# Kernel optimization log

Hardware: AMD Instinct MI355X
Metric: run time of the kernel (lower is better)

The kernel has to match this reference:

```python
import jax, jax.numpy as jnp
import numpy as np

B, C, T, F, H, O, L = 32, 8, 64, 256, 512, 1, 2


def _gru_layer(x, h0, Wih, Whh, bih, bhh):
    # x: [N, T, Fin]; Wih: [3H, Fin]; Whh: [3H, H]
    gi = jnp.einsum('ntf,gf->ntg', x, Wih) + bih  # precompute input gates [N, T, 3H]

    def step(h, gi_t):
        gh = h @ Whh.T + bhh                      # [N, 3H]
        ir, iz, inn = jnp.split(gi_t, 3, axis=-1)
        hr, hz, hn = jnp.split(gh, 3, axis=-1)
        r = jax.nn.sigmoid(ir + hr)
        z = jax.nn.sigmoid(iz + hz)
        n = jnp.tanh(inn + r * hn)
        h = (1.0 - z) * n + z * h                 # PyTorch GRU update
        return h, h

    hT, ys = jax.lax.scan(step, h0, jnp.swapaxes(gi, 0, 1))
    return jnp.swapaxes(ys, 0, 1), hT             # [N, T, H], [N, H]


def setup_inputs() -> dict:
    key = jax.random.key(0)
    ks = jax.random.split(key, 12)
    s = 1.0 / np.sqrt(H)
    u = lambda k, shp: jax.random.uniform(k, shp, jnp.float32, -s, s)
    return {
        'x': jax.random.normal(ks[0], (B, C, T, F), jnp.float32),
        'Wih0': u(ks[1], (3 * H, F)),
        'Whh0': u(ks[2], (3 * H, H)),
        'bih0': u(ks[3], (3 * H,)),
        'bhh0': u(ks[4], (3 * H,)),
        'Wih1': u(ks[5], (3 * H, H)),
        'Whh1': u(ks[6], (3 * H, H)),
        'bih1': u(ks[7], (3 * H,)),
        'bhh1': u(ks[8], (3 * H,)),
        'fcW': u(ks[9], (O, H)),
        'fcb': u(ks[10], (O,)),
    }


def reference(x, Wih0, Whh0, bih0, bhh0, Wih1, Whh1, bih1, bhh1, fcW, fcb):
    b, c, t, f = x.shape
    xf = x.reshape(b * c, t, f)
    h0 = jnp.zeros((b * c, H), x.dtype)
    # The per-timestep Python loop in the original carries h_n, which is
    # mathematically identical to a full-sequence GRU; out after the loop is
    # the top-layer output at the final timestep.
    y0, _ = _gru_layer(xf, h0, Wih0, Whh0, bih0, bhh0)
    y1, _ = _gru_layer(y0, h0, Wih1, Whh1, bih1, bhh1)
    last = y1[:, -1, :]                           # [b*c, H]
    out = last @ fcW.T + fcb                      # [b*c, O]
    out = out.reshape(b, c, -1).squeeze(axis=2)   # O == 1 -> [b, c]
    return jnp.mean(out, axis=1)                  # [b]
```

## Files before the change

### kernel.cpp

```cpp
#include <hip/hip_runtime.h>
#include <math.h>

#define BB 32
#define CC 8
#define TT 64
#define FF 256
#define HH 512
#define G3 1536
#define NSEQ 256
#define MROWS 16384

#define SGRP 16
#define NGRP 4

typedef _Float16 f16x8 __attribute__((ext_vector_type(8)));
typedef float f32x4 __attribute__((ext_vector_type(4)));

#define TMg 128
#define TNg 128
#define TKg 16

__global__ __launch_bounds__(256) void gemm_bias(
    const float* __restrict__ A, const float* __restrict__ W,
    const float* __restrict__ bias, float* __restrict__ C,
    int M, int N, int K)
{
  __shared__ float As[TKg][TMg + 4];
  __shared__ float Ws[TKg][TNg + 4];
  const int bm = blockIdx.y * TMg;
  const int bn = blockIdx.x * TNg;
  const int tid = threadIdx.x;
  const int tx = tid & 15;
  const int ty = tid >> 4;
  float acc[8][8];
#pragma unroll
  for (int i = 0; i < 8; ++i)
#pragma unroll
    for (int j = 0; j < 8; ++j) acc[i][j] = 0.f;

  for (int k0 = 0; k0 < K; k0 += TKg) {
    __syncthreads();
#pragma unroll
    for (int i = 0; i < 8; ++i) {
      int e = i * 256 + tid;
      int r = e >> 4;
      int c = e & 15;
      As[c][r] = A[(size_t)(bm + r) * K + (k0 + c)];
      Ws[c][r] = W[(size_t)(bn + r) * K + (k0 + c)];
    }
    __syncthreads();
#pragma unroll
    for (int k = 0; k < TKg; ++k) {
      float a[8], w[8];
#pragma unroll
      for (int i = 0; i < 8; ++i) a[i] = As[k][ty * 8 + i];
#pragma unroll
      for (int j = 0; j < 8; ++j) w[j] = Ws[k][tx + 16 * j];
#pragma unroll
      for (int i = 0; i < 8; ++i)
#pragma unroll
        for (int j = 0; j < 8; ++j) acc[i][j] = fmaf(a[i], w[j], acc[i][j]);
    }
  }
#pragma unroll
  for (int i = 0; i < 8; ++i) {
    size_t m = (size_t)(bm + ty * 8 + i);
#pragma unroll
    for (int j = 0; j < 8; ++j) {
      int n = bn + tx + 16 * j;
      C[m * N + n] = acc[i][j] + bias[n];
    }
  }
}

__global__ __launch_bounds__(256) void conv16(
    const float* __restrict__ x, _Float16* __restrict__ xh, int n8)
{
  int i = blockIdx.x * 256 + threadIdx.x;
  if (i < n8) {
    float4 a = reinterpret_cast<const float4*>(x)[i * 2];
    float4 b = reinterpret_cast<const float4*>(x)[i * 2 + 1];
    f16x8 v;
    v[0] = (_Float16)a.x; v[1] = (_Float16)a.y; v[2] = (_Float16)a.z; v[3] = (_Float16)a.w;
    v[4] = (_Float16)b.x; v[5] = (_Float16)b.y; v[6] = (_Float16)b.z; v[7] = (_Float16)b.w;
    reinterpret_cast<f16x8*>(xh)[i] = v;
  }
}

__global__ __launch_bounds__(256) void pack_wih(
    const float* __restrict__ W, _Float16* __restrict__ P, int K)
{
  int id = blockIdx.x * 256 + threadIdx.x;
  int lane = id & 63;
  int kcs = K >> 5;
  int t6 = id >> 6;
  int kc = t6 % kcs;
  int tile = t6 / kcs;
  if (tile >= 96) return;
  int row = tile * 16 + (lane & 15);
  int k0 = kc * 32 + ((lane >> 4) * 8);
  const float* src = W + (size_t)row * K + k0;
  f16x8 v;
#pragma unroll
  for (int i = 0; i < 8; ++i) v[i] = (_Float16)src[i];
  *reinterpret_cast<f16x8*>(P + (size_t)id * 8) = v;
}

__global__ __launch_bounds__(256) void pack_whh(
    const float* __restrict__ W, _Float16* __restrict__ P)
{
  int id = blockIdx.x * 256 + threadIdx.x;
  int lane = id & 63;
  int kc = (id >> 6) & 15;
  int tidx = id >> 10;
  int ng = tidx / 24;
  int tl = tidx % 24;
  int g = tl >> 3, sub = tl & 7;
  int gt = g * 32 + ng * 8 + sub;
  int row = gt * 16 + (lane & 15);
  int k0 = kc * 32 + ((lane >> 4) * 8);
  const float* src = W + (size_t)row * HH + k0;
  f16x8 v;
#pragma unroll
  for (int i = 0; i < 8; ++i) v[i] = (_Float16)src[i];
  *reinterpret_cast<f16x8*>(P + (size_t)id * 8) = v;
}

__device__ __forceinline__ void gload16g(const _Float16* g, _Float16* l) {
  __builtin_amdgcn_global_load_lds(
      (const __attribute__((address_space(1))) unsigned int*)g,
      (__attribute__((address_space(3))) unsigned int*)l, 16, 0, 0);
}

__global__ __launch_bounds__(256, 2) void gemm_mfma(
    const _Float16* __restrict__ A,
    const _Float16* __restrict__ Bp,
    const float* __restrict__ bias,
    float* __restrict__ C,
    int K)
{
  __shared__ __align__(16) _Float16 As[2][128][36];
  __shared__ __align__(16) _Float16 Bs[2][8 * 512];

  const int tid = threadIdx.x;
  const int lane = tid & 63;
  const int wv = tid >> 6;
  const int wm = wv >> 1, wn = wv & 1;
  const int bnT = blockIdx.x * 8;
  const int bm = blockIdx.y * 128;
  const int kcs = K >> 5;

  const int arow = lane & 15;
  const int agrp = lane >> 4;
  const int dcol = lane & 15;
  const int mrow = (lane >> 4) * 4;

  f32x4 acc[4][4];
#pragma unroll
  for (int i = 0; i < 4; ++i)
#pragma unroll
    for (int j = 0; j < 4; ++j) acc[i][j] = (f32x4){0.f, 0.f, 0.f, 0.f};

  auto stageA = [&](int s, int b) {
#pragma unroll
    for (int p = 0; p < 2; ++p) {
      int idx = p * 256 + tid;
      int row = idx >> 2;
      int cs = idx & 3;
      f16x8 v = *reinterpret_cast<const f16x8*>(
          A + (size_t)(bm + row) * K + s * 32 + cs * 8);
      *reinterpret_cast<f16x8*>(&As[b][row][cs * 8]) = v;
    }
  };
  auto stageB = [&](int s, int b) {
#pragma unroll
    for (int q = 0; q < 2; ++q) {
      int nt = wv * 2 + q;
      const _Float16* src = Bp + ((size_t)((bnT + nt) * kcs + s) * 64 + lane) * 8;
      gload16g(src, &Bs[b][nt * 512]);
    }
  };

  stageA(0, 0);
  stageB(0, 0);
  __syncthreads();

  for (int s = 0; s < kcs; ++s) {
    const int b = s & 1;
    if (s + 1 < kcs) {
      stageA(s + 1, b ^ 1);
      stageB(s + 1, b ^ 1);
    }
    f16x8 af[4], bf[4];
#pragma unroll
    for (int mt = 0; mt < 4; ++mt)
      af[mt] = *reinterpret_cast<const f16x8*>(&As[b][wm * 64 + mt * 16 + arow][agrp * 8]);
#pragma unroll
    for (int nt = 0; nt < 4; ++nt)
      bf[nt] = *reinterpret_cast<const f16x8*>(&Bs[b][(wn * 4 + nt) * 512 + lane * 8]);
#pragma unroll
    for (int mt = 0; mt < 4; ++mt)
#pragma unroll
      for (int nt = 0; nt < 4; ++nt)
        acc[mt][nt] = __builtin_amdgcn_mfma_f32_16x16x32_f16(af[mt], bf[nt], acc[mt][nt], 0, 0, 0);
    __syncthreads();
  }

#pragma unroll
  for (int nt = 0; nt < 4; ++nt) {
    const int n = (bnT + wn * 4 + nt) * 16 + dcol;
    const float bv = bias[n];
#pragma unroll
    for (int mt = 0; mt < 4; ++mt) {
      const size_t m0 = (size_t)(bm + wm * 64 + mt * 16 + mrow);
#pragma unroll
      for (int r = 0; r < 4; ++r)
        C[(m0 + r) * G3 + n] = acc[mt][nt][r] + bv;
    }
  }
}

#define SPB2 16
#define HSTR 520

#define LOADW(buf, g)                                                            \
  {                                                                              \
    const _Float16* _s = packW +                                                 \
        (((size_t)(ng * 24 + (g) * 8 + wid)) * 16) * 512 + (size_t)lane * 8;     \
    _Pragma("unroll")                                                            \
    for (int kc = 0; kc < 16; ++kc)                                              \
      buf[kc] = *reinterpret_cast<const f16x8*>(_s + (size_t)kc * 512);          \
  }

#define MF16(buf, acc)                                                           \
  {                                                                              \
    _Pragma("unroll")                                                            \
    for (int kc = 0; kc < 16; ++kc) {                                            \
      f16x8 _ha = *reinterpret_cast<const f16x8*>(&hs[arow][kc * 32 + agrp * 8]); \
      acc = __builtin_amdgcn_mfma_f32_16x16x32_f16(_ha, buf[kc], acc, 0, 0, 0);  \
    }                                                                            \
  }

__global__ __launch_bounds__(512, 1) void gru_scan_mfma(
    const float* __restrict__ gi,
    const _Float16* __restrict__ packW,
    const float* __restrict__ bhh,
    float* __restrict__ hfin,
    _Float16* __restrict__ yout,
    _Float16* __restrict__ hx,
    unsigned int* __restrict__ flags)
{
  __shared__ __align__(16) _Float16 hs[SPB2][HSTR];

  const int tid = threadIdx.x;
  const int lane = tid & 63;
  const int wid = tid >> 6;
  const int bid = blockIdx.x;
  const int sg = bid >> 2;
  const int ng = bid & 3;
  const int seq0 = sg * SPB2;

  const int arow = lane & 15;
  const int agrp = lane >> 4;
  const int dcol = lane & 15;
  const int mrow = (lane >> 4) * 4;

  const int cg = ng * 128 + wid * 16 + dcol;

  const float bhr = bhh[cg];
  const float bhz = bhh[HH + cg];
  const float bhn = bhh[2 * HH + cg];

  f16x8 wbR[16], wbZ[16], wbN[16];
  LOADW(wbR, 0)
  LOADW(wbZ, 1)
  LOADW(wbN, 2)

  float hold[4] = {0.f, 0.f, 0.f, 0.f};

  for (int e = tid; e < SPB2 * HSTR; e += 512)
    hs[e / HSTR][e % HSTR] = (_Float16)0.f;
  __syncthreads();

  for (int t = 0; t < TT; ++t) {
    float gir[4], giz[4], gin[4];
#pragma unroll
    for (int r = 0; r < 4; ++r) {
      const float* p0 = gi + ((size_t)(seq0 + mrow + r) * TT + t) * G3;
      gir[r] = p0[cg];
      giz[r] = p0[HH + cg];
      gin[r] = p0[2 * HH + cg];
    }

    if (t > 0) {
      if (tid < NGRP) {
        const unsigned int* fp = &flags[((size_t)sg * NGRP + tid) * TT + (t - 1)];
        while (__hip_atomic_load(fp, __ATOMIC_RELAXED, __HIP_MEMORY_SCOPE_AGENT) == 0u) {}
      }
      __syncthreads();
      {
        const _Float16* src = hx + (size_t)(t & 1) * NSEQ * HH
                              + (size_t)seq0 * HH + (size_t)tid * 16;
        f16x8 v0, v1;
        asm volatile(
            "global_load_dwordx4 %0, %2, off sc0 sc1\n\t"
            "global_load_dwordx4 %1, %2, off offset:16 sc0 sc1\n\t"
            "s_waitcnt vmcnt(0)"
            : "=&v"(v0), "=&v"(v1) : "v"(src) : "memory");
        int e0 = tid * 16;
        int row = e0 >> 9;
        int col = e0 & 511;
        *reinterpret_cast<f16x8*>(&hs[row][col]) = v0;
        *reinterpret_cast<f16x8*>(&hs[row][col + 8]) = v1;
      }
      __syncthreads();
    }

    f32x4 aR = {0.f,0.f,0.f,0.f}, aZ = {0.f,0.f,0.f,0.f}, aN = {0.f,0.f,0.f,0.f};
    MF16(wbR, aR)
    MF16(wbZ, aZ)
    MF16(wbN, aN)

    const int nb = (t + 1) & 1;
#pragma unroll
    for (int r = 0; r < 4; ++r) {
      float hr = aR[r] + bhr;
      float hz = aZ[r] + bhz;
      float hn = aN[r] + bhn;
      float rr = __builtin_amdgcn_rcpf(1.f + __expf(-(gir[r] + hr)));
      float zz = __builtin_amdgcn_rcpf(1.f + __expf(-(giz[r] + hz)));
      float ex = __expf(2.f * (gin[r] + rr * hn));
      float nn = 1.f - 2.f * __builtin_amdgcn_rcpf(ex + 1.f);
      float hnew = nn + zz * (hold[r] - nn);
      hold[r] = hnew;
      {
        _Float16 h16 = (_Float16)hnew;
        unsigned int hv32 = (unsigned int)__builtin_bit_cast(unsigned short, h16);
        _Float16* addr = hx + (size_t)nb * NSEQ * HH
                         + (size_t)(seq0 + mrow + r) * HH + cg;
        asm volatile("global_store_short %0, %1, off sc0 sc1"
                     :: "v"(addr), "v"(hv32) : "memory");
      }
      if (yout)
        yout[((size_t)(seq0 + mrow + r) * TT + t) * HH + cg] = (_Float16)hnew;
    }

    asm volatile("s_waitcnt vmcnt(0)" ::: "memory");
    __syncthreads();
    if (tid == 0)
      __hip_atomic_store(&flags[((size_t)sg * NGRP + ng) * TT + t], 1u,
                         __ATOMIC_RELAXED, __HIP_MEMORY_SCOPE_AGENT);
  }

#pragma unroll
  for (int r = 0; r < 4; ++r)
    hfin[(size_t)(seq0 + mrow + r) * HH + cg] = hold[r];
}

#define QS 4
#define SCTH 512
__global__ __launch_bounds__(SCTH) void gru_scan2f(
    const float* __restrict__ gi, const float* __restrict__ W,
    const float* __restrict__ bhh, float* __restrict__ hfin,
    float* __restrict__ yout)
{
  __shared__ __align__(16) float hsl[HH][QS];
  const int col = threadIdx.x;
  const int seq0 = blockIdx.x * QS;
  const float bh0 = bhh[col];
  const float bh1 = bhh[HH + col];
  const float bh2 = bhh[2 * HH + col];
  const float* w0p = W + (size_t)col * HH;
  const float* w1p = W + (size_t)(HH + col) * HH;
  const float* w2p = W + (size_t)(2 * HH + col) * HH;

  *reinterpret_cast<float4*>(&hsl[col][0]) = make_float4(0.f, 0.f, 0.f, 0.f);
  __syncthreads();

  for (int t = 0; t < TT; ++t) {
    float acc0[QS], acc1[QS], acc2[QS];
#pragma unroll
    for (int s = 0; s < QS; ++s) { acc0[s] = bh0; acc1[s] = bh1; acc2[s] = bh2; }
    float4 ho = *reinterpret_cast<const float4*>(&hsl[col][0]);
    float hold[QS] = {ho.x, ho.y, ho.z, ho.w};
#pragma unroll 2
    for (int k0 = 0; k0 < HH; k0 += 4) {
      float w[3][4];
      float4 a = *reinterpret_cast<const float4*>(&w0p[k0]);
      w[0][0] = a.x; w[0][1] = a.y; w[0][2] = a.z; w[0][3] = a.w;
      float4 b = *reinterpret_cast<const float4*>(&w1p[k0]);
      w[1][0] = b.x; w[1][1] = b.y; w[1][2] = b.z; w[1][3] = b.w;
      float4 c = *reinterpret_cast<const float4*>(&w2p[k0]);
      w[2][0] = c.x; w[2][1] = c.y; w[2][2] = c.z; w[2][3] = c.w;
#pragma unroll
      for (int kk = 0; kk < 4; ++kk) {
        float4 h4 = *reinterpret_cast<const float4*>(&hsl[k0 + kk][0]);
        float hq[4] = {h4.x, h4.y, h4.z, h4.w};
#pragma unroll
        for (int s = 0; s < QS; ++s) {
          acc0[s] = fmaf(hq[s], w[0][kk], acc0[s]);
          acc1[s] = fmaf(hq[s], w[1][kk], acc1[s]);
          acc2[s] = fmaf(hq[s], w[2][kk], acc2[s]);
        }
      }
    }
    __syncthreads();
    float hnew[QS];
#pragma unroll
    for (int s = 0; s < QS; ++s) {
      size_t grow = ((size_t)(seq0 + s) * TT + t) * G3;
      float ir = gi[grow + col];
      float iz = gi[grow + HH + col];
      float inn = gi[grow + 2 * HH + col];
      float r = 1.f / (1.f + expf(-(ir + acc0[s])));
      float z = 1.f / (1.f + expf(-(iz + acc1[s])));
      float nn = tanhf(inn + r * acc2[s]);
      hnew[s] = (1.f - z) * nn + z * hold[s];
      if (yout) yout[((size_t)(seq0 + s) * TT + t) * HH + col] = hnew[s];
    }
    *reinterpret_cast<float4*>(&hsl[col][0]) =
        make_float4(hnew[0], hnew[1], hnew[2], hnew[3]);
    __syncthreads();
  }
#pragma unroll
  for (int s = 0; s < QS; ++s)
    hfin[(size_t)(seq0 + s) * HH + col] = hsl[col][s];
}

__global__ __launch_bounds__(256) void fc_mean(
    const float* __restrict__ hfin, const float* __restrict__ fcW,
    const float* __restrict__ fcb, float* __restrict__ out)
{
  __shared__ float red[256];
  const int b = blockIdx.x;
  const int tid = threadIdx.x;
  float sum = 0.f;
  for (int e = tid; e < CC * HH; e += 256) {
    int c = e >> 9;
    int k = e & (HH - 1);
    sum += hfin[(size_t)(b * CC + c) * HH + k] * fcW[k];
  }
  red[tid] = sum;
  __syncthreads();
  for (int w = 128; w > 0; w >>= 1) {
    if (tid < w) red[tid] += red[tid + w];
    __syncthreads();
  }
  if (tid == 0) out[b] = red[0] * (1.f / CC) + fcb[0];
}

extern "C" void kernel_launch(void* const* d_in, const int* in_sizes, int n_in,
                              void* d_out, int out_size, void* d_ws, size_t ws_size,
                              hipStream_t stream)
{
  const float* x    = (const float*)d_in[0];
  const float* Wih0 = (const float*)d_in[1];
  const float* Whh0 = (const float*)d_in[2];
  const float* bih0 = (const float*)d_in[3];
  const float* bhh0 = (const float*)d_in[4];
  const float* Wih1 = (const float*)d_in[5];
  const float* Whh1 = (const float*)d_in[6];
  const float* bih1 = (const float*)d_in[7];
  const float* bhh1 = (const float*)d_in[8];
  const float* fcW  = (const float*)d_in[9];
  const float* fcb  = (const float*)d_in[10];
  float* out = (float*)d_out;

  char* ws = (char*)d_ws;
  float* gibuf = (float*)ws;
  _Float16* y0h  = (_Float16*)(ws + 100663296ull);
  _Float16* xh   = (_Float16*)(ws + 117440512ull);
  _Float16* pWih = (_Float16*)(ws + 125829120ull);
  _Float16* pWhh = (_Float16*)(ws + 127401984ull);
  _Float16* hx   = (_Float16*)(ws + 128974848ull);
  unsigned int* flags = (unsigned int*)(ws + 129499136ull);
  float* hfin = (float*)(ws + 134217728ull);
  float* y0f  = (float*)(ws + 100663296ull);
  const bool mfma_ok = (ws_size >= 134742016ull);

  if (mfma_ok) {
    conv16<<<dim3((MROWS * FF / 8 + 255) / 256), 256, 0, stream>>>(x, xh, MROWS * FF / 8);
    pack_wih<<<dim3(192), 256, 0, stream>>>(Wih0, pWih, FF);
    gemm_mfma<<<dim3(12, 128), 256, 0, stream>>>(xh, pWih, bih0, gibuf, FF);

    pack_whh<<<dim3(384), 256, 0, stream>>>(Whh0, pWhh);
    hipMemsetAsync(flags, 0, SGRP * NGRP * TT * sizeof(unsigned int), stream);
    gru_scan_mfma<<<dim3(SGRP * NGRP), 512, 0, stream>>>(gibuf, pWhh, bhh0, hfin, y0h, hx, flags);

    pack_wih<<<dim3(384), 256, 0, stream>>>(Wih1, pWih, HH);
    gemm_mfma<<<dim3(12, 128), 256, 0, stream>>>(y0h, pWih, bih1, gibuf, HH);

    pack_whh<<<dim3(384), 256, 0, stream>>>(Whh1, pWhh);
    hipMemsetAsync(flags, 0, SGRP * NGRP * TT * sizeof(unsigned int), stream);
    gru_scan_mfma<<<dim3(SGRP * NGRP), 512, 0, stream>>>(gibuf, pWhh, bhh1, hfin, nullptr, hx, flags);
  } else {
    gemm_bias<<<dim3(G3 / TNg, MROWS / TMg), 256, 0, stream>>>(x, Wih0, bih0, gibuf, MROWS, G3, FF);
    gru_scan2f<<<dim3(NSEQ / QS), SCTH, 0, stream>>>(gibuf, Whh0, bhh0, hfin, y0f);
    gemm_bias<<<dim3(G3 / TNg, MROWS / TMg), 256, 0, stream>>>(y0f, Wih1, bih1, gibuf, MROWS, G3, HH);
    gru_scan2f<<<dim3(NSEQ / QS), SCTH, 0, stream>>>(gibuf, Whh1, bhh1, hfin, nullptr);
  }

  fc_mean<<<dim3(BB), 256, 0, stream>>>(hfin, fcW, fcb, out);
}
```

Measured before the change: 623.8 us.

## Repartition GRU scan blocks into 4 sequence groups by 16 column groups with LDS weights

Changes the recurrent scan's work split from 16 sequence groups times 4 column groups to 4 sequence groups of 64 sequences times 16 column groups of 32 hidden units. Each block now keeps its 96 KB slice of packed Whh in LDS instead of in registers. Each wave loads its h operand fragments straight from global memory rather than staging them through shared memory, which removes one barrier per step. The trade-off is that each step must now wait on flags from 16 peer blocks instead of 4, and the weights are read from LDS on every step.

```diff
diff --git a/kernel.cpp b/kernel.cpp
--- a/kernel.cpp
+++ b/kernel.cpp
@@ -10,8 +10,8 @@
 #define NSEQ 256
 #define MROWS 16384
 
-#define SGRP 16
-#define NGRP 4
+#define SGB 4
+#define NGB 16
 
 typedef _Float16 f16x8 __attribute__((ext_vector_type(8)));
 typedef float f32x4 __attribute__((ext_vector_type(4)));
@@ -113,10 +113,10 @@
   int lane = id & 63;
   int kc = (id >> 6) & 15;
   int tidx = id >> 10;
-  int ng = tidx / 24;
-  int tl = tidx % 24;
-  int g = tl >> 3, sub = tl & 7;
-  int gt = g * 32 + ng * 8 + sub;
+  int ng = tidx / 6;
+  int tl = tidx % 6;
+  int g = tl >> 1, sub = tl & 1;
+  int gt = g * 32 + ng * 2 + sub;
   int row = gt * 16 + (lane & 15);
   int k0 = kc * 32 + ((lane >> 4) * 8);
   const float* src = W + (size_t)row * HH + k0;
@@ -220,26 +220,9 @@
   }
 }
 
-#define SPB2 16
-#define HSTR 520
-
-#define LOADW(buf, g)                                                            \
-  {                                                                              \
-    const _Float16* _s = packW +                                                 \
-        (((size_t)(ng * 24 + (g) * 8 + wid)) * 16) * 512 + (size_t)lane * 8;     \
-    _Pragma("unroll")                                                            \
-    for (int kc = 0; kc < 16; ++kc)                                              \
-      buf[kc] = *reinterpret_cast<const f16x8*>(_s + (size_t)kc * 512);          \
-  }
-
-#define MF16(buf, acc)                                                           \
-  {                                                                              \
-    _Pragma("unroll")                                                            \
-    for (int kc = 0; kc < 16; ++kc) {                                            \
-      f16x8 _ha = *reinterpret_cast<const f16x8*>(&hs[arow][kc * 32 + agrp * 8]); \
-      acc = __builtin_amdgcn_mfma_f32_16x16x32_f16(_ha, buf[kc], acc, 0, 0, 0);  \
-    }                                                                            \
-  }
+#define GLH(k, offs)                                                              \
+  asm volatile("global_load_dwordx4 %0, %1, off offset:" offs " sc0 sc1"          \
+               : "=&v"(af[k]) : "v"(hbase));
 
 __global__ __launch_bounds__(512, 1) void gru_scan_mfma(
     const float* __restrict__ gi,
@@ -250,78 +233,89 @@
     _Float16* __restrict__ hx,
     unsigned int* __restrict__ flags)
 {
-  __shared__ __align__(16) _Float16 hs[SPB2][HSTR];
+  __shared__ __align__(16) _Float16 wlds[6 * 16 * 64 * 8];
 
   const int tid = threadIdx.x;
   const int lane = tid & 63;
-  const int wid = tid >> 6;
+  const int w = tid >> 6;
   const int bid = blockIdx.x;
-  const int sg = bid >> 2;
-  const int ng = bid & 3;
-  const int seq0 = sg * SPB2;
-
-  const int arow = lane & 15;
+  const int sg = bid & 3;
+  const int ng = bid >> 2;
+  const int seq0 = sg * 64;
+
+  const int m = w >> 1;
+  const int p = w & 1;
+  const int arow16 = lane & 15;
   const int agrp = lane >> 4;
   const int dcol = lane & 15;
   const int mrow = (lane >> 4) * 4;
 
-  const int cg = ng * 128 + wid * 16 + dcol;
+  const int cg = ng * 32 + p * 16 + dcol;
+  const int seqm = seq0 + m * 16;
+
+  {
+    const _Float16* slice = packW + (size_t)ng * (6 * 16 * 64 * 8);
+#pragma unroll 4
+    for (int it = 0; it < 12; ++it) {
+      int blk = it * 8 + w;
+      gload16g(slice + (size_t)(blk * 64 + lane) * 8,
+               &wlds[(size_t)(blk * 64) * 8]);
+    }
+  }
 
   const float bhr = bhh[cg];
   const float bhz = bhh[HH + cg];
   const float bhn = bhh[2 * HH + cg];
 
-  f16x8 wbR[16], wbZ[16], wbN[16];
-  LOADW(wbR, 0)
-  LOADW(wbZ, 1)
-  LOADW(wbN, 2)
+  const int tR = p, tZ = 2 + p, tN = 4 + p;
 
   float hold[4] = {0.f, 0.f, 0.f, 0.f};
 
-  for (int e = tid; e < SPB2 * HSTR; e += 512)
-    hs[e / HSTR][e % HSTR] = (_Float16)0.f;
   __syncthreads();
 
   for (int t = 0; t < TT; ++t) {
+    const int cb = t & 1;
+    const int nb = cb ^ 1;
+
     float gir[4], giz[4], gin[4];
 #pragma unroll
     for (int r = 0; r < 4; ++r) {
-      const float* p0 = gi + ((size_t)(seq0 + mrow + r) * TT + t) * G3;
+      const float* p0 = gi + ((size_t)(seqm + mrow + r) * TT + t) * G3;
       gir[r] = p0[cg];
       giz[r] = p0[HH + cg];
       gin[r] = p0[2 * HH + cg];
     }
 
+    f32x4 aR = {0.f,0.f,0.f,0.f}, aZ = {0.f,0.f,0.f,0.f}, aN = {0.f,0.f,0.f,0.f};
+
     if (t > 0) {
-      if (tid < NGRP) {
-        const unsigned int* fp = &flags[((size_t)sg * NGRP + tid) * TT + (t - 1)];
+      if (tid < NGB) {
+        const unsigned int* fp = &flags[((size_t)sg * NGB + tid) * TT + (t - 1)];
         while (__hip_atomic_load(fp, __ATOMIC_RELAXED, __HIP_MEMORY_SCOPE_AGENT) == 0u) {}
       }
       __syncthreads();
-      {
-        const _Float16* src = hx + (size_t)(t & 1) * NSEQ * HH
-                              + (size_t)seq0 * HH + (size_t)tid * 16;
-        f16x8 v0, v1;
-        asm volatile(
-            "global_load_dwordx4 %0, %2, off sc0 sc1\n\t"
-            "global_load_dwordx4 %1, %2, off offset:16 sc0 sc1\n\t"
-            "s_waitcnt vmcnt(0)"
-            : "=&v"(v0), "=&v"(v1) : "v"(src) : "memory");
-        int e0 = tid * 16;
-        int row = e0 >> 9;
-        int col = e0 & 511;
-        *reinterpret_cast<f16x8*>(&hs[row][col]) = v0;
-        *reinterpret_cast<f16x8*>(&hs[row][col + 8]) = v1;
+
+      f16x8 af[16];
+      const _Float16* hbase = hx + (size_t)cb * NSEQ * HH
+                              + (size_t)(seqm + arow16) * HH + agrp * 8;
+      GLH(0, "0")    GLH(1, "64")   GLH(2, "128")  GLH(3, "192")
+      GLH(4, "256")  GLH(5, "320")  GLH(6, "384")  GLH(7, "448")
+      GLH(8, "512")  GLH(9, "576")  GLH(10, "640") GLH(11, "704")
+      GLH(12, "768") GLH(13, "832") GLH(14, "896") GLH(15, "960")
+      asm volatile("s_waitcnt vmcnt(0)" ::: "memory");
+      __builtin_amdgcn_sched_barrier(0);
+
+#pragma unroll
+      for (int kc = 0; kc < 16; ++kc) {
+        f16x8 br = *reinterpret_cast<const f16x8*>(&wlds[(size_t)((tR * 16 + kc) * 64 + lane) * 8]);
+        f16x8 bz = *reinterpret_cast<const f16x8*>(&wlds[(size_t)((tZ * 16 + kc) * 64 + lane) * 8]);
+        f16x8 bn = *reinterpret_cast<const f16x8*>(&wlds[(size_t)((tN * 16 + kc) * 64 + lane) * 8]);
+        aR = __builtin_amdgcn_mfma_f32_16x16x32_f16(af[kc], br, aR, 0, 0, 0);
+        aZ = __builtin_amdgcn_mfma_f32_16x16x32_f16(af[kc], bz, aZ, 0, 0, 0);
+        aN = __builtin_amdgcn_mfma_f32_16x16x32_f16(af[kc], bn, aN, 0, 0, 0);
       }
-      __syncthreads();
-    }
-
-    f32x4 aR = {0.f,0.f,0.f,0.f}, aZ = {0.f,0.f,0.f,0.f}, aN = {0.f,0.f,0.f,0.f};
-    MF16(wbR, aR)
-    MF16(wbZ, aZ)
-    MF16(wbN, aN)
-
-    const int nb = (t + 1) & 1;
+    }
+
 #pragma unroll
     for (int r = 0; r < 4; ++r) {
       float hr = aR[r] + bhr;
@@ -337,24 +331,24 @@
         _Float16 h16 = (_Float16)hnew;
         unsigned int hv32 = (unsigned int)__builtin_bit_cast(unsigned short, h16);
         _Float16* addr = hx + (size_t)nb * NSEQ * HH
-                         + (size_t)(seq0 + mrow + r) * HH + cg;
+                         + (size_t)(seqm + mrow + r) * HH + cg;
         asm volatile("global_store_short %0, %1, off sc0 sc1"
                      :: "v"(addr), "v"(hv32) : "memory");
       }
       if (yout)
-        yout[((size_t)(seq0 + mrow + r) * TT + t) * HH + cg] = (_Float16)hnew;
+        yout[((size_t)(seqm + mrow + r) * TT + t) * HH + cg] = (_Float16)hnew;
     }
 
     asm volatile("s_waitcnt vmcnt(0)" ::: "memory");
     __syncthreads();
     if (tid == 0)
-      __hip_atomic_store(&flags[((size_t)sg * NGRP + ng) * TT + t], 1u,
+      __hip_atomic_store(&flags[((size_t)sg * NGB + ng) * TT + t], 1u,
                          __ATOMIC_RELAXED, __HIP_MEMORY_SCOPE_AGENT);
   }
 
 #pragma unroll
   for (int r = 0; r < 4; ++r)
-    hfin[(size_t)(seq0 + mrow + r) * HH + cg] = hold[r];
+    hfin[(size_t)(seqm + mrow + r) * HH + cg] = hold[r];
 }
 
 #define QS 4
@@ -484,15 +478,15 @@
     gemm_mfma<<<dim3(12, 128), 256, 0, stream>>>(xh, pWih, bih0, gibuf, FF);
 
     pack_whh<<<dim3(384), 256, 0, stream>>>(Whh0, pWhh);
-    hipMemsetAsync(flags, 0, SGRP * NGRP * TT * sizeof(unsigned int), stream);
-    gru_scan_mfma<<<dim3(SGRP * NGRP), 512, 0, stream>>>(gibuf, pWhh, bhh0, hfin, y0h, hx, flags);
+    hipMemsetAsync(flags, 0, SGB * NGB * TT * sizeof(unsigned int), stream);
+    gru_scan_mfma<<<dim3(SGB * NGB), 512, 0, stream>>>(gibuf, pWhh, bhh0, hfin, y0h, hx, flags);
 
     pack_wih<<<dim3(384), 256, 0, stream>>>(Wih1, pWih, HH);
     gemm_mfma<<<dim3(12, 128), 256, 0, stream>>>(y0h, pWih, bih1, gibuf, HH);
 
     pack_whh<<<dim3(384), 256, 0, stream>>>(Whh1, pWhh);
-    hipMemsetAsync(flags, 0, SGRP * NGRP * TT * sizeof(unsigned int), stream);
-    gru_scan_mfma<<<dim3(SGRP * NGRP), 512, 0, stream>>>(gibuf, pWhh, bhh1, hfin, nullptr, hx, flags);
+    hipMemsetAsync(flags, 0, SGB * NGB * TT * sizeof(unsigned int), stream);
+    gru_scan_mfma<<<dim3(SGB * NGB), 512, 0, stream>>>(gibuf, pWhh, bhh1, hfin, nullptr, hx, flags);
   } else {
     gemm_bias<<<dim3(G3 / TNg, MROWS / TMg), 256, 0, stream>>>(x, Wih0, bih0, gibuf, MROWS, G3, FF);
     gru_scan2f<<<dim3(NSEQ / QS), SCTH, 0, stream>>>(gibuf, Whh0, bhh0, hfin, y0f);
```

Result: slower. 875.2 us (+40.3%).
